# Performance work log

Measured on AMD Instinct MI355X. Metric: run time of the kernel, lower is better.

Reference implementation:

```python
import jax, jax.numpy as jnp
import numpy as np

DIM = 1024
NUM_HEADS = 16
HEAD_DIM = DIM // NUM_HEADS  # 64
H = 32
W = 32
NREG = 8
B = 8
N = H * W + NREG  # 1032


def setup_inputs() -> dict:
    key = jax.random.key(0)
    ks = jax.random.split(key, 6)
    def rn(k, shape, std):
        return jax.random.normal(k, shape, dtype=jnp.float32) * std
    return {
        "x": rn(ks[0], (B, N, DIM), 1.0),
        "qkv_w": rn(ks[1], (3 * DIM, DIM), 0.02),
        "qkv_b": jnp.zeros((3 * DIM,), jnp.float32),
        "proj_w": rn(ks[2], (DIM, DIM), 0.02),
        "proj_b": jnp.zeros((DIM,), jnp.float32),
        "rel_pos_h": rn(ks[3], (2 * H - 1, HEAD_DIM), 0.02),
        "rel_pos_w": rn(ks[4], (2 * W - 1, HEAD_DIM), 0.02),
        "nreg": NREG,
        "cait": 0,
    }


def _rel_pos_table(rel_pos, size):
    # q_size == k_size == size -> relative index = i - j + (size - 1)
    coords = jnp.arange(size)[:, None] - jnp.arange(size)[None, :] + (size - 1)
    return rel_pos[coords]  # (size, size, head_dim)


def reference(x, qkv_w, qkv_b, proj_w, proj_b, rel_pos_h, rel_pos_w, nreg, cait):
    Bx, Nx, C = x.shape
    hd = C // NUM_HEADS
    scale = hd ** (-0.5)
    # qkv: (B, N, 3, nH, hd) -> (3, nH, B, N, hd) -> (3, nH*B, N, hd)
    qkv = (x @ qkv_w.T + qkv_b).reshape(Bx, Nx, 3, NUM_HEADS, hd)
    qkv = jnp.transpose(qkv, (2, 3, 0, 1, 4)).reshape(3, NUM_HEADS * Bx, Nx, hd)
    q, k, v = qkv[0], qkv[1], qkv[2]
    if cait:
        q = q[:, -nreg:]
    attn = jnp.einsum('bqd,bkd->bqk', q * scale, k)  # (nH*B, Nq, N)
    if not cait:
        hw = H * W
        Rh = _rel_pos_table(rel_pos_h, H)  # (H, H, hd)
        Rw = _rel_pos_table(rel_pos_w, W)  # (W, W, hd)
        r_q = q[:, :hw].reshape(-1, H, W, hd)  # unscaled q, grid tokens only
        rel_h = jnp.einsum('bhwc,hkc->bhwk', r_q, Rh)
        rel_w = jnp.einsum('bhwc,wkc->bhwk', r_q, Rw)
        grid = (attn[:, :hw, :hw].reshape(-1, H, W, H, W)
                + rel_h[:, :, :, :, None] + rel_w[:, :, :, None, :])
        attn = attn.at[:, :hw, :hw].set(grid.reshape(-1, hw, hw))
    attn = jax.nn.softmax(attn, axis=-1)
    out = jnp.einsum('bqk,bkd->bqd', attn, v)  # (nH*B, Nq, hd)
    out = out.reshape(NUM_HEADS, Bx, -1, hd)
    out = jnp.transpose(out, (1, 2, 0, 3)).reshape(Bx, -1, C)
    return out @ proj_w.T + proj_b
```

## Files before the change

### kernel.cpp

```cpp
#include <hip/hip_runtime.h>

#define BATCH 8
#define NTOK 1032
#define NPAD 1152
#define MTOT (BATCH*NTOK)
#define MPAD 8320

#define SCALE_Q 0.18033688011112042f
#define C2      5.770780163555854f

typedef __bf16 bf16x8 __attribute__((ext_vector_type(8)));
typedef float f32x4 __attribute__((ext_vector_type(4)));
typedef unsigned short us8 __attribute__((ext_vector_type(8)));
typedef unsigned short us4 __attribute__((ext_vector_type(4)));
typedef short s4 __attribute__((ext_vector_type(4)));

__device__ __forceinline__ unsigned short f2bf(float f){
  unsigned int u = __builtin_bit_cast(unsigned int, f);
  u += 0x7fffu + ((u >> 16) & 1u);
  return (unsigned short)(u >> 16);
}
__device__ __forceinline__ float bf2f(unsigned short u){
  return __builtin_bit_cast(float, (unsigned int)u << 16);
}

#define MFMA16(a,b,c) __builtin_amdgcn_mfma_f32_16x16x32_bf16( \
    __builtin_bit_cast(bf16x8,(a)), __builtin_bit_cast(bf16x8,(b)), (c), 0, 0, 0)
#define MFMAH(a,b,c) __builtin_amdgcn_mfma_f32_16x16x16bf16_1k( \
    __builtin_bit_cast(s4,(a)), __builtin_bit_cast(s4,(b)), (c), 0, 0, 0)

__device__ __forceinline__ void gl_lds16(const unsigned short* g, unsigned short* l){
  __builtin_amdgcn_global_load_lds(
      (const __attribute__((address_space(1))) unsigned int*)g,
      (__attribute__((address_space(3))) unsigned int*)l, 16, 0, 0);
}

__global__ __launch_bounds__(256) void cvt_f32_bf16(const float* __restrict__ in,
                                                    unsigned short* __restrict__ out, int n4){
  int i = blockIdx.x * 256 + threadIdx.x;
  if (i < n4){
    float4 v = reinterpret_cast<const float4*>(in)[i];
    us4 o; o.x = f2bf(v.x); o.y = f2bf(v.y); o.z = f2bf(v.z); o.w = f2bf(v.w);
    reinterpret_cast<us4*>(out)[i] = o;
  }
}

__global__ __launch_bounds__(256) void pad_zero(unsigned short* __restrict__ qb,
                                                unsigned short* __restrict__ kb,
                                                unsigned short* __restrict__ vt,
                                                unsigned short* __restrict__ xb,
                                                unsigned short* __restrict__ ao){
  int i = blockIdx.x * 256 + threadIdx.x;
  const int t1 = 128 * (NPAD - NTOK) * 64;
  const int t2 = t1 + (MPAD - MTOT) * 1024;
  const int t3 = t2 + (MPAD - MTOT) * 1024;
  if (i < t1){
    int bh = i / ((NPAD - NTOK) * 64);
    int r  = (i / 64) % (NPAD - NTOK);
    int d  = i % 64;
    int idx = (bh * NPAD + NTOK + r) * 64 + d;
    qb[idx] = 0;
    kb[idx] = 0;
    vt[(bh * 64 + d) * NPAD + NTOK + r] = 0;
  } else if (i < t2){
    xb[(size_t)MTOT * 1024 + (i - t1)] = 0;
  } else if (i < t3){
    ao[(size_t)MTOT * 1024 + (i - t2)] = 0;
  }
}

__global__ __launch_bounds__(256,2) void qkv_gemm(
    const unsigned short* __restrict__ A,
    const unsigned short* __restrict__ Bw,
    const float* __restrict__ bias,
    unsigned short* __restrict__ qb,
    unsigned short* __restrict__ kb,
    unsigned short* __restrict__ vt)
{
  const int K = 1024;
  __shared__ __align__(16) unsigned short As[128*32];
  __shared__ __align__(16) unsigned short Bs[128*32];
  int tid = threadIdx.x;
  int id = blockIdx.x;
  int work = (id & 7) * 195 + (id >> 3);
  int m0 = (work / 24) * 128, n0 = (work % 24) * 128;
  int w = tid >> 6, lane = tid & 63, lr = lane & 15, lg = lane >> 4;
  int wr = w >> 1, wc = w & 1;
  int srow = lane >> 2, scol = (lane & 3) * 8;
  f32x4 acc[4][4] = {};

  for (int k0 = 0; k0 < K; k0 += 32){
    __syncthreads();
    #pragma unroll
    for (int i = 0; i < 2; i++){
      int q = w * 2 + i;
      gl_lds16(&A [(size_t)(m0 + q*16 + srow) * K + k0 + scol], &As[q*512]);
      gl_lds16(&Bw[(size_t)(n0 + q*16 + srow) * K + k0 + scol], &Bs[q*512]);
    }
    __syncthreads();
    us8 a[4], b[4];
    #pragma unroll
    for (int mi = 0; mi < 4; mi++) a[mi] = *reinterpret_cast<const us8*>(&As[(wr*64 + mi*16 + lr)*32 + lg*8]);
    #pragma unroll
    for (int ni = 0; ni < 4; ni++) b[ni] = *reinterpret_cast<const us8*>(&Bs[(wc*64 + ni*16 + lr)*32 + lg*8]);
    #pragma unroll
    for (int mi = 0; mi < 4; mi++)
      #pragma unroll
      for (int ni = 0; ni < 4; ni++)
        acc[mi][ni] = MFMA16(a[mi], b[ni], acc[mi][ni]);
  }

  #pragma unroll
  for (int mi = 0; mi < 4; mi++){
    #pragma unroll
    for (int ni = 0; ni < 4; ni++){
      #pragma unroll
      for (int reg = 0; reg < 4; reg++){
        int m = m0 + wr*64 + mi*16 + lg*4 + reg;
        if (m >= MTOT) continue;
        int n = n0 + wc*64 + ni*16 + lr;
        float val = acc[mi][ni][reg] + bias[n];
        int b_ = m / NTOK, nidx = m % NTOK;
        int t = n >> 10, h = (n >> 6) & 15, d = n & 63;
        int bh = h * BATCH + b_;
        if (t == 0){
          qb[(size_t)(bh * NPAD + nidx) * 64 + d] = f2bf(val * SCALE_Q);
        } else if (t == 1){
          kb[(size_t)(bh * NPAD + nidx) * 64 + d] = f2bf(val);
        } else {
          vt[(size_t)(bh * 64 + d) * NPAD + nidx] = f2bf(val);
        }
      }
    }
  }
}

__global__ __launch_bounds__(256,3) void attn_kernel(
    const unsigned short* __restrict__ qb,
    const unsigned short* __restrict__ kb,
    const unsigned short* __restrict__ vt,
    const float* __restrict__ rph,
    const float* __restrict__ rpw,
    unsigned short* __restrict__ ao)
{
  __shared__ __align__(16) unsigned short Ks[2][64*64];
  __shared__ __align__(16) unsigned short Vs[2][64*64];
  __shared__ unsigned short RHt[32*128];
  __shared__ unsigned short RWc[32*128];

  int id = blockIdx.x;
  int work = (id & 7) * 144 + (id >> 3);
  int bh = work / 9;
  int qt = work % 9;
  int tid = threadIdx.x, w = tid >> 6, lane = tid & 63, lr = lane & 15, lg = lane >> 4;
  int h = bh >> 3, b_ = bh & 7;

  const unsigned short* qbase = qb + (size_t)bh * NPAD * 64;
  const unsigned short* kbase = kb + (size_t)bh * NPAD * 64;
  const unsigned short* vbase = vt + (size_t)bh * 64 * NPAD;

  #pragma unroll
  for (int t = 0; t < 2; t++){
    int i = t*256 + tid;
    int row = i >> 3, cs = (i & 7) ^ (row & 7);
    gl_lds16(&kbase[(size_t)row*64 + cs*8],   &Ks[0][(t*256 + w*64)*8]);
    gl_lds16(&vbase[(size_t)row*NPAD + cs*8], &Vs[0][(t*256 + w*64)*8]);
  }

  us8 aq[2][2];
  #pragma unroll
  for (int qf = 0; qf < 2; qf++){
    int qrow = qt*128 + w*32 + qf*16 + lr;
    aq[qf][0] = *reinterpret_cast<const us8*>(&qbase[(size_t)qrow*64 + lg*8]);
    aq[qf][1] = *reinterpret_cast<const us8*>(&qbase[(size_t)qrow*64 + 32 + lg*8]);
  }

  float rwreg[2][2][4] = {};

  if (qt < 8){
    int qh = qt*4 + w;
    f32x4 accH[2][2] = {};
    #pragma unroll
    for (int ks = 0; ks < 2; ks++){
      #pragma unroll
      for (int nf2 = 0; nf2 < 2; nf2++){
        int t = nf2*16 + lr;
        const float* src = rph + (size_t)(qh - t + 31)*64 + ks*32 + lg*8;
        us8 ar;
        #pragma unroll
        for (int j = 0; j < 8; j++) ar[j] = f2bf(src[j]);
        #pragma unroll
        for (int qf = 0; qf < 2; qf++) accH[qf][nf2] = MFMA16(ar, aq[qf][ks], accH[qf][nf2]);
      }
    }
    #pragma unroll
    for (int qf = 0; qf < 2; qf++)
      #pragma unroll
      for (int nf2 = 0; nf2 < 2; nf2++)
        #pragma unroll
        for (int reg = 0; reg < 4; reg++){
          int t_out = nf2*16 + lg*4 + reg;
          RHt[t_out*128 + w*32 + qf*16 + lr] = f2bf(accH[qf][nf2][reg] * 8.0f);
        }
    f32x4 accW[2][4] = {};
    #pragma unroll
    for (int ks = 0; ks < 2; ks++){
      #pragma unroll
      for (int nf = 0; nf < 4; nf++){
        int t = nf*16 + lr;
        us8 aw_ = {};
        if (t < 63){
          const float* src = rpw + (size_t)t*64 + ks*32 + lg*8;
          #pragma unroll
          for (int j = 0; j < 8; j++) aw_[j] = f2bf(src[j]);
        }
        #pragma unroll
        for (int qf = 0; qf < 2; qf++) accW[qf][nf] = MFMA16(aw_, aq[qf][ks], accW[qf][nf]);
      }
    }
    #pragma unroll
    for (int qf = 0; qf < 2; qf++)
      #pragma unroll
      for (int nf = 0; nf < 4; nf++)
        #pragma unroll
        for (int reg = 0; reg < 4; reg++){
          int t_out = nf*16 + lg*4 + reg;
          int qw = qf*16 + lr;
          int kw = qw - t_out + 31;
          if (kw >= 0 && kw < 32)
            RWc[kw*128 + w*32 + qf*16 + lr] = f2bf(accW[qf][nf][reg] * 8.0f);
        }
    #pragma unroll
    for (int qf = 0; qf < 2; qf++)
      #pragma unroll
      for (int hf = 0; hf < 2; hf++)
        #pragma unroll
        for (int reg = 0; reg < 4; reg++)
          rwreg[qf][hf][reg] = bf2f(RWc[(hf*16 + lg*4 + reg)*128 + w*32 + qf*16 + lr]);
  }
  __syncthreads();

  f32x4 O[2][4] = {};
  f32x4 lac[2] = {};
  s4 ones4;
  ones4.x = (short)0x3F80; ones4.y = (short)0x3F80; ones4.z = (short)0x3F80; ones4.w = (short)0x3F80;

  for (int kt = 0; kt < 17; kt++){
    int cur = kt & 1;
    if (kt < 16){
      #pragma unroll
      for (int t = 0; t < 2; t++){
        int i = t*256 + tid;
        int row = i >> 3, cs = (i & 7) ^ (row & 7);
        gl_lds16(&kbase[(size_t)((kt+1)*64 + row)*64 + cs*8], &Ks[cur^1][(t*256 + w*64)*8]);
        gl_lds16(&vbase[(size_t)row*NPAD + (kt+1)*64 + cs*8], &Vs[cur^1][(t*256 + w*64)*8]);
      }
    }

    f32x4 S[2][4] = {};
    __builtin_amdgcn_s_setprio(1);
    #pragma unroll
    for (int ks = 0; ks < 2; ks++)
      #pragma unroll
      for (int nf = 0; nf < 4; nf++){
        us8 bk = *reinterpret_cast<const us8*>(
            &Ks[cur][(nf*16 + lr)*64 + (((ks*4 + lg) ^ (lr & 7)) * 8)]);
        S[0][nf] = MFMA16(bk, aq[0][ks], S[0][nf]);
        S[1][nf] = MFMA16(bk, aq[1][ks], S[1][nf]);
      }
    __builtin_amdgcn_s_setprio(0);

    bool gk = (qt < 8) && (kt < 16);
    float rh2[2][2];
    #pragma unroll
    for (int qf = 0; qf < 2; qf++)
      #pragma unroll
      for (int hf = 0; hf < 2; hf++)
        rh2[qf][hf] = gk ? (bf2f(RHt[(kt*2 + hf)*128 + w*32 + qf*16 + lr]) - C2) : -C2;

    s4 pa[2][4];
    #pragma unroll
    for (int qf = 0; qf < 2; qf++){
      #pragma unroll
      for (int nf = 0; nf < 4; nf++){
        float pv[4];
        #pragma unroll
        for (int reg = 0; reg < 4; reg++){
          float logit = S[qf][nf][reg] + rh2[qf][nf>>1] + (gk ? rwreg[qf][nf&1][reg] : 0.f);
          float p = __builtin_amdgcn_exp2f(logit);
          int key = kt*64 + nf*16 + lg*4 + reg;
          pv[reg] = (key < NTOK) ? p : 0.f;
        }
        unsigned int u0 = __builtin_amdgcn_perm(
            __builtin_bit_cast(unsigned int, pv[1]), __builtin_bit_cast(unsigned int, pv[0]), 0x07060302u);
        unsigned int u1 = __builtin_amdgcn_perm(
            __builtin_bit_cast(unsigned int, pv[3]), __builtin_bit_cast(unsigned int, pv[2]), 0x07060302u);
        uint2 uu; uu.x = u0; uu.y = u1;
        pa[qf][nf] = __builtin_bit_cast(s4, uu);
      }
    }

    __builtin_amdgcn_s_setprio(1);
    #pragma unroll
    for (int qf = 0; qf < 2; qf++)
      #pragma unroll
      for (int nf = 0; nf < 4; nf++)
        lac[qf] = MFMAH(pa[qf][nf], ones4, lac[qf]);
    #pragma unroll
    for (int nf = 0; nf < 4; nf++){
      #pragma unroll
      for (int nfd = 0; nfd < 4; nfd++){
        us4 bv = *reinterpret_cast<const us4*>(
            &Vs[cur][(nfd*16 + lr)*64 + (((nf*2 + (lg>>1)) ^ (lr & 7))*8) + (lg&1)*4]);
        O[0][nfd] = MFMAH(pa[0][nf], bv, O[0][nfd]);
        O[1][nfd] = MFMAH(pa[1][nf], bv, O[1][nfd]);
      }
    }
    __builtin_amdgcn_s_setprio(0);
    __syncthreads();
  }

  #pragma unroll
  for (int qf = 0; qf < 2; qf++)
    #pragma unroll
    for (int reg = 0; reg < 4; reg++){
      int qg = qt*128 + w*32 + qf*16 + lg*4 + reg;
      if (qg < NTOK){
        float inv = 1.0f / lac[qf][reg];
        #pragma unroll
        for (int nfd = 0; nfd < 4; nfd++)
          ao[(size_t)(b_ * NTOK + qg) * 1024 + h*64 + nfd*16 + lr] = f2bf(O[qf][nfd][reg] * inv);
      }
    }
}

__global__ __launch_bounds__(256,2) void proj_gemm(
    const unsigned short* __restrict__ A,
    const unsigned short* __restrict__ Bw,
    const float* __restrict__ bias,
    float* __restrict__ out)
{
  const int K = 1024;
  __shared__ __align__(16) unsigned short As[128*32];
  __shared__ __align__(16) unsigned short Bs[128*32];
  int tid = threadIdx.x;
  int id = blockIdx.x;
  int work = (id & 7) * 65 + (id >> 3);
  int m0 = (work / 8) * 128, n0 = (work % 8) * 128;
  int w = tid >> 6, lane = tid & 63, lr = lane & 15, lg = lane >> 4;
  int wr = w >> 1, wc = w & 1;
  int srow = lane >> 2, scol = (lane & 3) * 8;
  f32x4 acc[4][4] = {};

  for (int k0 = 0; k0 < K; k0 += 32){
    __syncthreads();
    #pragma unroll
    for (int i = 0; i < 2; i++){
      int q = w * 2 + i;
      gl_lds16(&A [(size_t)(m0 + q*16 + srow) * K + k0 + scol], &As[q*512]);
      gl_lds16(&Bw[(size_t)(n0 + q*16 + srow) * K + k0 + scol], &Bs[q*512]);
    }
    __syncthreads();
    us8 a[4], b[4];
    #pragma unroll
    for (int mi = 0; mi < 4; mi++) a[mi] = *reinterpret_cast<const us8*>(&As[(wr*64 + mi*16 + lr)*32 + lg*8]);
    #pragma unroll
    for (int ni = 0; ni < 4; ni++) b[ni] = *reinterpret_cast<const us8*>(&Bs[(wc*64 + ni*16 + lr)*32 + lg*8]);
    #pragma unroll
    for (int mi = 0; mi < 4; mi++)
      #pragma unroll
      for (int ni = 0; ni < 4; ni++)
        acc[mi][ni] = MFMA16(a[mi], b[ni], acc[mi][ni]);
  }

  #pragma unroll
  for (int mi = 0; mi < 4; mi++){
    #pragma unroll
    for (int ni = 0; ni < 4; ni++){
      #pragma unroll
      for (int reg = 0; reg < 4; reg++){
        int m = m0 + wr*64 + mi*16 + lg*4 + reg;
        if (m >= MTOT) continue;
        int n = n0 + wc*64 + ni*16 + lr;
        out[(size_t)m * 1024 + n] = acc[mi][ni][reg] + bias[n];
      }
    }
  }
}

extern "C" void kernel_launch(void* const* d_in, const int* in_sizes, int n_in,
                              void* d_out, int out_size, void* d_ws, size_t ws_size,
                              hipStream_t stream)
{
  const float* x      = (const float*)d_in[0];
  const float* qkv_w  = (const float*)d_in[1];
  const float* qkv_b  = (const float*)d_in[2];
  const float* proj_w = (const float*)d_in[3];
  const float* proj_b = (const float*)d_in[4];
  const float* rph    = (const float*)d_in[5];
  const float* rpw    = (const float*)d_in[6];
  float* out = (float*)d_out;

  char* ws = (char*)d_ws;
  size_t off = 0;
  auto alloc = [&](size_t bytes){ char* p = ws + off; off += (bytes + 255) & ~(size_t)255; return p; };
  unsigned short* x_bf  = (unsigned short*)alloc((size_t)MPAD * 1024 * 2);
  unsigned short* qw_bf = (unsigned short*)alloc((size_t)3072 * 1024 * 2);
  unsigned short* pw_bf = (unsigned short*)alloc((size_t)1024 * 1024 * 2);
  unsigned short* qbuf  = (unsigned short*)alloc((size_t)128 * NPAD * 64 * 2);
  unsigned short* kbuf  = (unsigned short*)alloc((size_t)128 * NPAD * 64 * 2);
  unsigned short* vtbuf = (unsigned short*)alloc((size_t)128 * 64 * NPAD * 2);
  unsigned short* aout  = (unsigned short*)alloc((size_t)MPAD * 1024 * 2);
  if (off > ws_size) return;

  int n4x = MTOT * 1024 / 4;
  cvt_f32_bf16<<<dim3((n4x + 255) / 256), 256, 0, stream>>>(x, x_bf, n4x);
  int n4q = 3072 * 1024 / 4;
  cvt_f32_bf16<<<dim3((n4q + 255) / 256), 256, 0, stream>>>(qkv_w, qw_bf, n4q);
  int n4p = 1024 * 1024 / 4;
  cvt_f32_bf16<<<dim3((n4p + 255) / 256), 256, 0, stream>>>(proj_w, pw_bf, n4p);

  int npad = 128 * (NPAD - NTOK) * 64 + 2 * (MPAD - MTOT) * 1024;
  pad_zero<<<dim3((npad + 255) / 256), 256, 0, stream>>>(qbuf, kbuf, vtbuf, x_bf, aout);

  qkv_gemm<<<dim3(1560), 256, 0, stream>>>(x_bf, qw_bf, qkv_b, qbuf, kbuf, vtbuf);
  attn_kernel<<<dim3(1152), 256, 0, stream>>>(qbuf, kbuf, vtbuf, rph, rpw, aout);
  proj_gemm<<<dim3(520), 256, 0, stream>>>(aout, pw_bf, proj_b, out);
}
```

Baseline: 241.1 us.

## Double-buffer GEMM LDS tiles and write V token-major with separate transpose

Both GEMMs now double-buffer their LDS A/B tiles, prefetching the next k-slice while computing the current one, and use one barrier per iteration instead of two; launch bounds rise to three blocks per CU. The qkv epilogue writes V in token-major layout (coalesced along d) into the aout buffer instead of strided transposed stores. A new transpose_v kernel then builds the padded V^T through LDS, zeroing the pad columns. This trades an extra launch and an extra pass over V for coalesced epilogue stores and overlapped loads. It relies on aout being overwritten by attention after V is consumed.

```diff
diff --git a/kernel.cpp b/kernel.cpp
--- a/kernel.cpp
+++ b/kernel.cpp
@@ -47,7 +47,6 @@
 
 __global__ __launch_bounds__(256) void pad_zero(unsigned short* __restrict__ qb,
                                                 unsigned short* __restrict__ kb,
-                                                unsigned short* __restrict__ vt,
                                                 unsigned short* __restrict__ xb,
                                                 unsigned short* __restrict__ ao){
   int i = blockIdx.x * 256 + threadIdx.x;
@@ -61,7 +60,6 @@
     int idx = (bh * NPAD + NTOK + r) * 64 + d;
     qb[idx] = 0;
     kb[idx] = 0;
-    vt[(bh * 64 + d) * NPAD + NTOK + r] = 0;
   } else if (i < t2){
     xb[(size_t)MTOT * 1024 + (i - t1)] = 0;
   } else if (i < t3){
@@ -69,17 +67,17 @@
   }
 }
 
-__global__ __launch_bounds__(256,2) void qkv_gemm(
+__global__ __launch_bounds__(256,3) void qkv_gemm(
     const unsigned short* __restrict__ A,
     const unsigned short* __restrict__ Bw,
     const float* __restrict__ bias,
     unsigned short* __restrict__ qb,
     unsigned short* __restrict__ kb,
-    unsigned short* __restrict__ vt)
+    unsigned short* __restrict__ vb)
 {
   const int K = 1024;
-  __shared__ __align__(16) unsigned short As[128*32];
-  __shared__ __align__(16) unsigned short Bs[128*32];
+  __shared__ __align__(16) unsigned short As[2][128*32];
+  __shared__ __align__(16) unsigned short Bs[2][128*32];
   int tid = threadIdx.x;
   int id = blockIdx.x;
   int work = (id & 7) * 195 + (id >> 3);
@@ -89,25 +87,36 @@
   int srow = lane >> 2, scol = (lane & 3) * 8;
   f32x4 acc[4][4] = {};
 
-  for (int k0 = 0; k0 < K; k0 += 32){
-    __syncthreads();
-    #pragma unroll
-    for (int i = 0; i < 2; i++){
-      int q = w * 2 + i;
-      gl_lds16(&A [(size_t)(m0 + q*16 + srow) * K + k0 + scol], &As[q*512]);
-      gl_lds16(&Bw[(size_t)(n0 + q*16 + srow) * K + k0 + scol], &Bs[q*512]);
-    }
-    __syncthreads();
+  #pragma unroll
+  for (int i = 0; i < 2; i++){
+    int q = w * 2 + i;
+    gl_lds16(&A [(size_t)(m0 + q*16 + srow) * K + scol], &As[0][q*512]);
+    gl_lds16(&Bw[(size_t)(n0 + q*16 + srow) * K + scol], &Bs[0][q*512]);
+  }
+  __syncthreads();
+
+  for (int kt = 0; kt < 32; kt++){
+    int cur = kt & 1;
+    if (kt < 31){
+      int k0 = (kt + 1) * 32;
+      #pragma unroll
+      for (int i = 0; i < 2; i++){
+        int q = w * 2 + i;
+        gl_lds16(&A [(size_t)(m0 + q*16 + srow) * K + k0 + scol], &As[cur^1][q*512]);
+        gl_lds16(&Bw[(size_t)(n0 + q*16 + srow) * K + k0 + scol], &Bs[cur^1][q*512]);
+      }
+    }
     us8 a[4], b[4];
     #pragma unroll
-    for (int mi = 0; mi < 4; mi++) a[mi] = *reinterpret_cast<const us8*>(&As[(wr*64 + mi*16 + lr)*32 + lg*8]);
-    #pragma unroll
-    for (int ni = 0; ni < 4; ni++) b[ni] = *reinterpret_cast<const us8*>(&Bs[(wc*64 + ni*16 + lr)*32 + lg*8]);
+    for (int mi = 0; mi < 4; mi++) a[mi] = *reinterpret_cast<const us8*>(&As[cur][(wr*64 + mi*16 + lr)*32 + lg*8]);
+    #pragma unroll
+    for (int ni = 0; ni < 4; ni++) b[ni] = *reinterpret_cast<const us8*>(&Bs[cur][(wc*64 + ni*16 + lr)*32 + lg*8]);
     #pragma unroll
     for (int mi = 0; mi < 4; mi++)
       #pragma unroll
       for (int ni = 0; ni < 4; ni++)
         acc[mi][ni] = MFMA16(a[mi], b[ni], acc[mi][ni]);
+    __syncthreads();
   }
 
   #pragma unroll
@@ -128,10 +137,39 @@
         } else if (t == 1){
           kb[(size_t)(bh * NPAD + nidx) * 64 + d] = f2bf(val);
         } else {
-          vt[(size_t)(bh * 64 + d) * NPAD + nidx] = f2bf(val);
+          vb[(size_t)(bh * NTOK + nidx) * 64 + d] = f2bf(val);
         }
       }
     }
+  }
+}
+
+__global__ __launch_bounds__(256) void transpose_v(const unsigned short* __restrict__ vb,
+                                                   unsigned short* __restrict__ vt){
+  __shared__ unsigned short Ls[64][72];
+  int blk = blockIdx.x;
+  int bh = blk / 17, tl = blk % 17;
+  int n0 = tl * 64;
+  int t = threadIdx.x;
+
+  #pragma unroll
+  for (int p = 0; p < 2; p++){
+    int idx = p * 256 + t;
+    int r = idx >> 3, c = idx & 7;
+    us8 v = {};
+    if (n0 + r < NTOK)
+      v = *reinterpret_cast<const us8*>(&vb[((size_t)bh * NTOK + n0 + r) * 64 + c * 8]);
+    *reinterpret_cast<us8*>(&Ls[r][c * 8]) = v;
+  }
+  __syncthreads();
+
+  int d = t & 63, ng = t >> 6;
+  us8 o[2];
+  #pragma unroll
+  for (int hf = 0; hf < 2; hf++){
+    #pragma unroll
+    for (int j = 0; j < 8; j++) o[hf][j] = Ls[ng*16 + hf*8 + j][d];
+    *reinterpret_cast<us8*>(&vt[((size_t)bh * 64 + d) * NPAD + n0 + ng*16 + hf*8]) = o[hf];
   }
 }
 
@@ -334,15 +372,15 @@
     }
 }
 
-__global__ __launch_bounds__(256,2) void proj_gemm(
+__global__ __launch_bounds__(256,3) void proj_gemm(
     const unsigned short* __restrict__ A,
     const unsigned short* __restrict__ Bw,
     const float* __restrict__ bias,
     float* __restrict__ out)
 {
   const int K = 1024;
-  __shared__ __align__(16) unsigned short As[128*32];
-  __shared__ __align__(16) unsigned short Bs[128*32];
+  __shared__ __align__(16) unsigned short As[2][128*32];
+  __shared__ __align__(16) unsigned short Bs[2][128*32];
   int tid = threadIdx.x;
   int id = blockIdx.x;
   int work = (id & 7) * 65 + (id >> 3);
@@ -352,25 +390,36 @@
   int srow = lane >> 2, scol = (lane & 3) * 8;
   f32x4 acc[4][4] = {};
 
-  for (int k0 = 0; k0 < K; k0 += 32){
-    __syncthreads();
-    #pragma unroll
-    for (int i = 0; i < 2; i++){
-      int q = w * 2 + i;
-      gl_lds16(&A [(size_t)(m0 + q*16 + srow) * K + k0 + scol], &As[q*512]);
-      gl_lds16(&Bw[(size_t)(n0 + q*16 + srow) * K + k0 + scol], &Bs[q*512]);
-    }
-    __syncthreads();
+  #pragma unroll
+  for (int i = 0; i < 2; i++){
+    int q = w * 2 + i;
+    gl_lds16(&A [(size_t)(m0 + q*16 + srow) * K + scol], &As[0][q*512]);
+    gl_lds16(&Bw[(size_t)(n0 + q*16 + srow) * K + scol], &Bs[0][q*512]);
+  }
+  __syncthreads();
+
+  for (int kt = 0; kt < 32; kt++){
+    int cur = kt & 1;
+    if (kt < 31){
+      int k0 = (kt + 1) * 32;
+      #pragma unroll
+      for (int i = 0; i < 2; i++){
+        int q = w * 2 + i;
+        gl_lds16(&A [(size_t)(m0 + q*16 + srow) * K + k0 + scol], &As[cur^1][q*512]);
+        gl_lds16(&Bw[(size_t)(n0 + q*16 + srow) * K + k0 + scol], &Bs[cur^1][q*512]);
+      }
+    }
     us8 a[4], b[4];
     #pragma unroll
-    for (int mi = 0; mi < 4; mi++) a[mi] = *reinterpret_cast<const us8*>(&As[(wr*64 + mi*16 + lr)*32 + lg*8]);
-    #pragma unroll
-    for (int ni = 0; ni < 4; ni++) b[ni] = *reinterpret_cast<const us8*>(&Bs[(wc*64 + ni*16 + lr)*32 + lg*8]);
+    for (int mi = 0; mi < 4; mi++) a[mi] = *reinterpret_cast<const us8*>(&As[cur][(wr*64 + mi*16 + lr)*32 + lg*8]);
+    #pragma unroll
+    for (int ni = 0; ni < 4; ni++) b[ni] = *reinterpret_cast<const us8*>(&Bs[cur][(wc*64 + ni*16 + lr)*32 + lg*8]);
     #pragma unroll
     for (int mi = 0; mi < 4; mi++)
       #pragma unroll
       for (int ni = 0; ni < 4; ni++)
         acc[mi][ni] = MFMA16(a[mi], b[ni], acc[mi][ni]);
+    __syncthreads();
   }
 
   #pragma unroll
@@ -413,6 +462,8 @@
   unsigned short* aout  = (unsigned short*)alloc((size_t)MPAD * 1024 * 2);
   if (off > ws_size) return;
 
+  unsigned short* vbuf = aout;
+
   int n4x = MTOT * 1024 / 4;
   cvt_f32_bf16<<<dim3((n4x + 255) / 256), 256, 0, stream>>>(x, x_bf, n4x);
   int n4q = 3072 * 1024 / 4;
@@ -421,9 +472,10 @@
   cvt_f32_bf16<<<dim3((n4p + 255) / 256), 256, 0, stream>>>(proj_w, pw_bf, n4p);
 
   int npad = 128 * (NPAD - NTOK) * 64 + 2 * (MPAD - MTOT) * 1024;
-  pad_zero<<<dim3((npad + 255) / 256), 256, 0, stream>>>(qbuf, kbuf, vtbuf, x_bf, aout);
-
-  qkv_gemm<<<dim3(1560), 256, 0, stream>>>(x_bf, qw_bf, qkv_b, qbuf, kbuf, vtbuf);
+  pad_zero<<<dim3((npad + 255) / 256), 256, 0, stream>>>(qbuf, kbuf, x_bf, aout);
+
+  qkv_gemm<<<dim3(1560), 256, 0, stream>>>(x_bf, qw_bf, qkv_b, qbuf, kbuf, vbuf);
+  transpose_v<<<dim3(128 * 17), 256, 0, stream>>>(vbuf, vtbuf);
   attn_kernel<<<dim3(1152), 256, 0, stream>>>(qbuf, kbuf, vtbuf, rph, rpw, aout);
   proj_gemm<<<dim3(520), 256, 0, stream>>>(aout, pw_bf, proj_b, out);
 }
```

Measured after the change: 230.9 us. -4.2%, faster.
